# Performance work log

Hardware: AMD Instinct MI355X
Metric: run time of the kernel (lower is better)

Reference implementation:

```python
import jax, jax.numpy as jnp
import numpy as np

WINDOW = 512
OVERLAP = 64
STRIDE = WINDOW - OVERLAP  # 448
HEADS = 12
HEAD_DIM = 3072 // HEADS  # 256
SCALE = 1.0 / np.sqrt(HEAD_DIM)


def setup_inputs() -> dict:
    key = jax.random.key(0)
    ks = jax.random.split(key, 9)
    B, S, H = 1, 8192, 3072
    w = 0.02  # weight init scale
    return {
        "hidden_states": jax.random.normal(ks[0], (B, S, H), jnp.float32),
        "Wq": jax.random.normal(ks[1], (H, H), jnp.float32) * w,
        "bq": jnp.zeros((H,), jnp.float32),
        "Wk": jax.random.normal(ks[2], (H, H), jnp.float32) * w,
        "bk": jnp.zeros((H,), jnp.float32),
        "Wv": jax.random.normal(ks[3], (H, H), jnp.float32) * w,
        "bv": jnp.zeros((H,), jnp.float32),
        "Wo": jax.random.normal(ks[4], (H, H), jnp.float32) * w,
        "bo": jnp.zeros((H,), jnp.float32),
    }


def reference(hidden_states, Wq, bq, Wk, bk, Wv, bv, Wo, bo):
    B, S, H = hidden_states.shape
    n_win = -(-S // STRIDE)  # ceil: windows start at 0, STRIDE, 2*STRIDE, ... < S
    starts = np.arange(n_win) * STRIDE                      # static
    idx = starts[:, None] + np.arange(WINDOW)[None, :]      # [n_win, W]
    valid = jnp.asarray(idx < S)                            # [n_win, W] bool
    idx_c = np.minimum(idx, S - 1)                          # clamp for gather

    # Gather overlapping windows: [B, n_win, W, H] (redundant QKV on overlap, as in original)
    win = hidden_states[:, idx_c]

    def proj(Wm, bm):
        y = jnp.einsum('bnwh,oh->bnwo', win, Wm) + bm
        return y.reshape(B, n_win, WINDOW, HEADS, HEAD_DIM)

    q = proj(Wq, bq)
    k = proj(Wk, bk)
    v = proj(Wv, bv)

    scores = jnp.einsum('bnqhd,bnkhd->bnhqk', q, k) * SCALE  # [B,n_win,heads,W,W]
    # Padded (out-of-range) key positions of the short last window must not attend
    scores = jnp.where(valid[None, :, None, None, :], scores, -1e9)
    attn = jax.nn.softmax(scores, axis=-1)
    ctx = jnp.einsum('bnhqk,bnkhd->bnqhd', attn, v)
    ctx = ctx.reshape(B, n_win, WINDOW, H)
    out_w = jnp.einsum('bnwh,oh->bnwo', ctx, Wo) + bo        # [B,n_win,W,H]

    # zero padded query rows, then overlap-add + average
    out_w = out_w * valid[None, :, :, None].astype(out_w.dtype)
    flat_idx = jnp.asarray(idx_c.reshape(-1))                # [n_win*W]
    output = jnp.zeros((B, S, H), out_w.dtype).at[:, flat_idx].add(
        out_w.reshape(B, -1, H))
    counts = jnp.zeros((S,), out_w.dtype).at[flat_idx].add(
        valid.reshape(-1).astype(out_w.dtype))
    return output / jnp.maximum(counts, 1.0)[None, :, None]
```

## Files before the change

kernel.cpp:

```cpp
#include <hip/hip_runtime.h>
#include <hip/hip_bf16.h>
#include <stdint.h>

#define SEQ   8192
#define HDIM  3072
#define NWIN  19
#define WINL  512
#define STR   448
#define NHEAD 12
#define DHEAD 256
#define QKVN  9216
#define KVB   32
#define ATTN_SCALE 0.0625f

typedef unsigned short u16;
typedef __bf16 bf16x8 __attribute__((ext_vector_type(8)));
typedef float  f32x4  __attribute__((ext_vector_type(4)));
typedef unsigned short us8 __attribute__((ext_vector_type(8)));

__device__ __forceinline__ u16 f2b(float x) {
  return __builtin_bit_cast(u16, __float2bfloat16(x));
}
__device__ __forceinline__ float b2f(u16 u) {
  return __builtin_bit_cast(float, (unsigned int)(u) << 16);
}
__device__ __forceinline__ void gload_lds16(const void* g, void* l) {
  __builtin_amdgcn_global_load_lds(
      (const __attribute__((address_space(1))) void*)g,
      (__attribute__((address_space(3))) void*)l, 16, 0, 0);
}

__global__ __launch_bounds__(256) void cvt_f32_bf16(const float* __restrict__ src,
                                                    u16* __restrict__ dst, int n8) {
  int i = blockIdx.x * 256 + threadIdx.x;
  if (i >= n8) return;
  const float4* s4 = (const float4*)src;
  float4 a = s4[2 * i], b = s4[2 * i + 1];
  us8 o;
  o[0] = f2b(a.x); o[1] = f2b(a.y); o[2] = f2b(a.z); o[3] = f2b(a.w);
  o[4] = f2b(b.x); o[5] = f2b(b.y); o[6] = f2b(b.z); o[7] = f2b(b.w);
  *((us8*)dst + i) = o;
}

__global__ __launch_bounds__(256) void biascat(const float* __restrict__ bq,
                                               const float* __restrict__ bk,
                                               const float* __restrict__ bv,
                                               float* __restrict__ dst) {
  int i = blockIdx.x * 256 + threadIdx.x;
  if (i >= QKVN) return;
  dst[i] = (i < HDIM) ? bq[i] : ((i < 2 * HDIM) ? bk[i - HDIM] : bv[i - 2 * HDIM]);
}

template <bool BF16OUT>
__global__ __launch_bounds__(512, 2) void gemm256(const u16* __restrict__ A,
                                                  const u16* __restrict__ B,
                                                  const float* __restrict__ bias,
                                                  float* __restrict__ outF,
                                                  u16* __restrict__ outB,
                                                  u16* __restrict__ vtOut,
                                                  int N, int K) {
  __shared__ __align__(16) u16 As[2][2][128][64];
  __shared__ __align__(16) u16 Bs[2][2][128][64];
  const int tid = threadIdx.x;
  const int w = tid >> 6, l = tid & 63;
  const int wm = w >> 2, wn = w & 3;
  const int fr = l & 15, g = l >> 4;
  const int xcd = blockIdx.x & 7, loc = blockIdx.x >> 3;
  const int bn = loc >> 2, bm = xcd * 4 + (loc & 3);

  const int srow = tid >> 3;
  const int lc = (tid & 7) ^ ((tid >> 3) & 7);
  const u16* sA0 = A + (size_t)(bm * 256 + srow) * K + lc * 8;
  const u16* sA1 = sA0 + (size_t)64 * K;
  const u16* sB0 = B + (size_t)(bn * 256 + srow) * K + lc * 8;
  const u16* sB1 = sB0 + (size_t)64 * K;
  const size_t hiK = (size_t)128 * K;
  const int t16 = tid * 16;
  char* Aw = (char*)As;
  char* Bw = (char*)Bs;

  int rbA[4], rbB[2], ck[2];
#pragma unroll
  for (int i = 0; i < 4; ++i) rbA[i] = (i * 32 + wm * 16 + fr) * 128;
  rbB[0] = (wn * 16 + fr) * 128;
  rbB[1] = (64 + wn * 16 + fr) * 128;
  ck[0] = ((g) ^ (fr & 7)) * 16;
  ck[1] = ((4 + g) ^ (fr & 7)) * 16;

  f32x4 acc[8][4];
#pragma unroll
  for (int i = 0; i < 8; ++i)
#pragma unroll
    for (int j = 0; j < 4; ++j) acc[i][j] = (f32x4){0.f, 0.f, 0.f, 0.f};

  gload_lds16(sA0, Aw + t16); gload_lds16(sA1, Aw + 8192 + t16);
  gload_lds16(sB0, Bw + t16); gload_lds16(sB1, Bw + 8192 + t16);
  gload_lds16(sB0 + hiK, Bw + 16384 + t16); gload_lds16(sB1 + hiK, Bw + 16384 + 8192 + t16);
  gload_lds16(sA0 + hiK, Aw + 16384 + t16); gload_lds16(sA1 + hiK, Aw + 16384 + 8192 + t16);
  sA0 += 64; sA1 += 64; sB0 += 64; sB1 += 64;
  asm volatile("s_waitcnt vmcnt(4)" ::: "memory");
  __builtin_amdgcn_s_barrier();
  __builtin_amdgcn_sched_barrier(0);

  const int NT = K >> 6;
  for (int T = 0; T < NT; ++T) {
    const int cur = T & 1, pp = (T + 1) & 1;
    const bool ds = (T + 1 < NT);
    const bool last = (T == NT - 1);
    const char* ah = (const char*)As + cur * 32768;
    const char* bh = (const char*)Bs + cur * 32768;
    char* apw = Aw + pp * 32768;
    char* bpw = Bw + pp * 32768;
    bf16x8 af[4][2], bf[4][2];

#pragma unroll
    for (int mi = 0; mi < 4; ++mi)
#pragma unroll
      for (int kk = 0; kk < 2; ++kk)
        af[mi][kk] = *(const bf16x8*)(ah + rbA[mi] + ck[kk]);
#pragma unroll
    for (int ni = 0; ni < 2; ++ni)
#pragma unroll
      for (int kk = 0; kk < 2; ++kk)
        bf[ni][kk] = *(const bf16x8*)(bh + rbB[ni] + ck[kk]);
    if (ds) { gload_lds16(sA0, apw + t16); gload_lds16(sA1, apw + 8192 + t16); }
    __builtin_amdgcn_s_barrier();
    asm volatile("s_waitcnt lgkmcnt(0)" ::: "memory");
    __builtin_amdgcn_sched_barrier(0);
    __builtin_amdgcn_s_setprio(1);
#pragma unroll
    for (int kk = 0; kk < 2; ++kk)
#pragma unroll
      for (int mi = 0; mi < 4; ++mi)
#pragma unroll
        for (int ni = 0; ni < 2; ++ni)
          acc[mi][ni] = __builtin_amdgcn_mfma_f32_16x16x32_bf16(af[mi][kk], bf[ni][kk], acc[mi][ni], 0, 0, 0);
    __builtin_amdgcn_s_setprio(0);
    if (last) asm volatile("s_waitcnt vmcnt(2)" ::: "memory");
    else      asm volatile("s_waitcnt vmcnt(4)" ::: "memory");
    __builtin_amdgcn_s_barrier();

#pragma unroll
    for (int ni = 2; ni < 4; ++ni)
#pragma unroll
      for (int kk = 0; kk < 2; ++kk)
        bf[ni][kk] = *(const bf16x8*)(bh + 16384 + rbB[ni - 2] + ck[kk]);
    if (ds) { gload_lds16(sB0, bpw + t16); gload_lds16(sB1, bpw + 8192 + t16); }
    __builtin_amdgcn_s_barrier();
    asm volatile("s_waitcnt lgkmcnt(0)" ::: "memory");
    __builtin_amdgcn_sched_barrier(0);
    __builtin_amdgcn_s_setprio(1);
#pragma unroll
    for (int kk = 0; kk < 2; ++kk)
#pragma unroll
      for (int mi = 0; mi < 4; ++mi)
#pragma unroll
        for (int ni = 2; ni < 4; ++ni)
          acc[mi][ni] = __builtin_amdgcn_mfma_f32_16x16x32_bf16(af[mi][kk], bf[ni][kk], acc[mi][ni], 0, 0, 0);
    __builtin_amdgcn_s_setprio(0);
    if (last) asm volatile("s_waitcnt vmcnt(0)" ::: "memory");
    else      asm volatile("s_waitcnt vmcnt(4)" ::: "memory");
    __builtin_amdgcn_s_barrier();

#pragma unroll
    for (int mi = 0; mi < 4; ++mi)
#pragma unroll
      for (int kk = 0; kk < 2; ++kk)
        af[mi][kk] = *(const bf16x8*)(ah + 16384 + rbA[mi] + ck[kk]);
    if (ds) { gload_lds16(sB0 + hiK, bpw + 16384 + t16); gload_lds16(sB1 + hiK, bpw + 16384 + 8192 + t16); }
    __builtin_amdgcn_s_barrier();
    asm volatile("s_waitcnt lgkmcnt(0)" ::: "memory");
    __builtin_amdgcn_sched_barrier(0);
    __builtin_amdgcn_s_setprio(1);
#pragma unroll
    for (int kk = 0; kk < 2; ++kk)
#pragma unroll
      for (int mi = 0; mi < 4; ++mi)
#pragma unroll
        for (int ni = 0; ni < 2; ++ni)
          acc[mi + 4][ni] = __builtin_amdgcn_mfma_f32_16x16x32_bf16(af[mi][kk], bf[ni][kk], acc[mi + 4][ni], 0, 0, 0);
    __builtin_amdgcn_s_setprio(0);
    __builtin_amdgcn_s_barrier();

    if (ds) { gload_lds16(sA0 + hiK, apw + 16384 + t16); gload_lds16(sA1 + hiK, apw + 16384 + 8192 + t16); }
    __builtin_amdgcn_s_barrier();
    __builtin_amdgcn_s_setprio(1);
#pragma unroll
    for (int kk = 0; kk < 2; ++kk)
#pragma unroll
      for (int mi = 0; mi < 4; ++mi)
#pragma unroll
        for (int ni = 2; ni < 4; ++ni)
          acc[mi + 4][ni] = __builtin_amdgcn_mfma_f32_16x16x32_bf16(af[mi][kk], bf[ni][kk], acc[mi + 4][ni], 0, 0, 0);
    __builtin_amdgcn_s_setprio(0);
    if (!last) asm volatile("s_waitcnt vmcnt(4)" ::: "memory");
    __builtin_amdgcn_s_barrier();
    if (ds) { sA0 += 64; sA1 += 64; sB0 += 64; sB1 += 64; }
    __builtin_amdgcn_sched_barrier(0);
  }

#pragma unroll
  for (int ni = 0; ni < 4; ++ni) {
    const int c = bn * 256 + ni * 64 + wn * 16 + fr;
    const float bvv = bias ? bias[c] : 0.0f;
    const bool wv = BF16OUT && (vtOut != nullptr) && (c >= 2 * HDIM);
#pragma unroll
    for (int mi = 0; mi < 8; ++mi) {
      const int r0 = bm * 256 + mi * 32 + wm * 16 + g * 4;
      u16 t4[4];
#pragma unroll
      for (int jj = 0; jj < 4; ++jj) {
        float v = acc[mi][ni][jj] + bvv;
        if (BF16OUT) { u16 b_ = f2b(v); outB[(size_t)(r0 + jj) * N + c] = b_; t4[jj] = b_; }
        else         outF[(size_t)(r0 + jj) * N + c] = v;
      }
      if (wv) *(uint2*)(vtOut + (size_t)(c - 2 * HDIM) * SEQ + r0) = *(const uint2*)t4;
    }
  }
}

__global__ __launch_bounds__(256, 2) void attn_kernel(const u16* __restrict__ QKV,
                                                      const u16* __restrict__ Vt,
                                                      u16* __restrict__ ctxw) {
  __shared__ __align__(16) u16 Ks[2][KVB * 256];
  __shared__ __align__(16) u16 Vs[2][256 * KVB];
  __shared__ __align__(16) u16 Ps[4][16 * KVB];
  const int qb = blockIdx.x, h = blockIdx.y, n = blockIdx.z;
  const int tid = threadIdx.x, w = tid >> 6, l = tid & 63;
  const int g = l >> 4, fr = l & 15;
  const int s0 = n * STR;

  bf16x8 qf[8];
  {
    int sq = s0 + qb * 64 + w * 16 + fr;
    if (sq > SEQ - 1) sq = SEQ - 1;
    const u16* qbase = QKV + (size_t)sq * QKVN + h * DHEAD + g * 8;
#pragma unroll
    for (int dc = 0; dc < 8; ++dc) qf[dc] = *(const bf16x8*)(qbase + dc * 32);
  }
  f32x4 ctx[16];
#pragma unroll
  for (int dn = 0; dn < 16; ++dn) ctx[dn] = (f32x4){0.f, 0.f, 0.f, 0.f};
  float mrow[4] = {-3e38f, -3e38f, -3e38f, -3e38f};
  float lrow[4] = {0.f, 0.f, 0.f, 0.f};

  auto stage = [&](int kt) {
    const int sb = s0 + kt * KVB;
#pragma unroll
    for (int i = 0; i < 4; ++i) {
      const int c = i * 4 + w;
      {
        const int krow = c * 2 + (l >> 5);
        const int cl = (l & 31) ^ krow;
        int sk = sb + krow;
        if (sk > SEQ - 1) sk = SEQ - 1;
        gload_lds16(QKV + (size_t)sk * QKVN + HDIM + h * DHEAD + cl * 8,
                    (char*)&Ks[kt & 1][0] + c * 1024);
      }
      {
        const int d = c * 16 + (l >> 2);
        const int cl = (l & 3) ^ (d & 3) ^ ((d >> 2) & 3);
        int sv = sb + cl * 8;
        if (sv > SEQ - 8) sv = SEQ - 8;
        gload_lds16(Vt + (size_t)(h * DHEAD + d) * SEQ + sv,
                    (char*)&Vs[kt & 1][0] + c * 1024);
      }
    }
  };

  stage(0);
  const int mv = (fr & 3) ^ ((fr >> 2) & 3);
  char* pw = (char*)&Ps[w][0];

  for (int kt = 0; kt < 16; ++kt) {
    asm volatile("s_waitcnt vmcnt(0)" ::: "memory");
    __builtin_amdgcn_s_barrier();
    __builtin_amdgcn_sched_barrier(0);
    if (kt + 1 < 16) stage(kt + 1);
    const char* kb = (const char*)&Ks[kt & 1][0];
    const char* vb = (const char*)&Vs[kt & 1][0];
    const int sb = s0 + kt * KVB;

    f32x4 sacc[2];
#pragma unroll
    for (int kn = 0; kn < 2; ++kn) sacc[kn] = (f32x4){0.f, 0.f, 0.f, 0.f};
#pragma unroll
    for (int kn = 0; kn < 2; ++kn) {
      const int krow = kn * 16 + fr;
      const char* krp = kb + krow * 512;
#pragma unroll
      for (int dc = 0; dc < 8; ++dc) {
        bf16x8 kf = *(const bf16x8*)(krp + (((dc * 4 + g) ^ krow) << 4));
        sacc[kn] = __builtin_amdgcn_mfma_f32_16x16x32_bf16(qf[dc], kf, sacc[kn], 0, 0, 0);
      }
    }
    float mt[4];
#pragma unroll
    for (int kn = 0; kn < 2; ++kn) {
      const bool valid = (sb + kn * 16 + fr) < SEQ;
#pragma unroll
      for (int r = 0; r < 4; ++r) {
        float v = valid ? sacc[kn][r] * ATTN_SCALE : -1e9f;
        sacc[kn][r] = v;
        mt[r] = (kn == 0) ? v : fmaxf(mt[r], v);
      }
    }
#pragma unroll
    for (int r = 0; r < 4; ++r) {
#pragma unroll
      for (int off = 1; off < 16; off <<= 1)
        mt[r] = fmaxf(mt[r], __shfl_xor(mt[r], off, 64));
    }
    float corr[4];
#pragma unroll
    for (int r = 0; r < 4; ++r) {
      float mnew = fmaxf(mrow[r], mt[r]);
      corr[r] = __expf(mrow[r] - mnew);
      mrow[r] = mnew;
    }
    float psum[4] = {0.f, 0.f, 0.f, 0.f};
#pragma unroll
    for (int kn = 0; kn < 2; ++kn) {
#pragma unroll
      for (int r = 0; r < 4; ++r) {
        float p = __expf(sacc[kn][r] - mrow[r]);
        psum[r] += p;
        const int q = g * 4 + r;
        const int kv = kn * 16 + fr;
        *(u16*)(pw + q * 64 + ((((kv >> 3) ^ r ^ g) << 4) | ((2 * kv) & 15))) = f2b(p);
      }
    }
#pragma unroll
    for (int r = 0; r < 4; ++r) {
#pragma unroll
      for (int off = 1; off < 16; off <<= 1)
        psum[r] += __shfl_xor(psum[r], off, 64);
      lrow[r] = lrow[r] * corr[r] + psum[r];
    }
#pragma unroll
    for (int dn = 0; dn < 16; ++dn)
#pragma unroll
      for (int r = 0; r < 4; ++r) ctx[dn][r] *= corr[r];

    bf16x8 pf = *(const bf16x8*)(pw + fr * 64 + ((g ^ mv) << 4));
#pragma unroll
    for (int dn = 0; dn < 16; ++dn) {
      const int d = dn * 16 + fr;
      bf16x8 vf = *(const bf16x8*)(vb + d * 64 + ((g ^ mv) << 4));
      ctx[dn] = __builtin_amdgcn_mfma_f32_16x16x32_bf16(pf, vf, ctx[dn], 0, 0, 0);
    }
  }
  float inv[4];
#pragma unroll
  for (int r = 0; r < 4; ++r) inv[r] = 1.0f / lrow[r];
  const int qrow0 = qb * 64 + w * 16 + g * 4;
#pragma unroll
  for (int dn = 0; dn < 16; ++dn) {
#pragma unroll
    for (int r = 0; r < 4; ++r) {
      ctxw[(size_t)(n * WINL + qrow0 + r) * HDIM + h * DHEAD + dn * 16 + fr] =
          f2b(ctx[dn][r] * inv[r]);
    }
  }
}

__global__ __launch_bounds__(256) void combine_kernel(const u16* __restrict__ ctxw,
                                                      u16* __restrict__ ctx_avg) {
  int idx = blockIdx.x * 256 + threadIdx.x;
  if (idx >= SEQ * (HDIM / 8)) return;
  const int s = idx / (HDIM / 8);
  const int cc = (idx % (HDIM / 8)) * 8;
  const int w1 = s / STR;
  const int off1 = s - w1 * STR;
  us8 a = *(const us8*)(ctxw + (size_t)(w1 * WINL + off1) * HDIM + cc);
  if (w1 >= 1 && off1 < (WINL - STR)) {
    us8 b = *(const us8*)(ctxw + (size_t)((w1 - 1) * WINL + off1 + STR) * HDIM + cc);
#pragma unroll
    for (int j = 0; j < 8; ++j) a[j] = f2b(0.5f * (b2f(a[j]) + b2f(b[j])));
  }
  *(us8*)(ctx_avg + (size_t)s * HDIM + cc) = a;
}

__global__ void ws_marker(float* out, float v) { out[0] = v; }

extern "C" void kernel_launch(void* const* d_in, const int* in_sizes, int n_in,
                              void* d_out, int out_size, void* d_ws, size_t ws_size,
                              hipStream_t stream) {
  const float* X  = (const float*)d_in[0];
  const float* Wq = (const float*)d_in[1];
  const float* bq = (const float*)d_in[2];
  const float* Wk = (const float*)d_in[3];
  const float* bk = (const float*)d_in[4];
  const float* Wv = (const float*)d_in[5];
  const float* bv = (const float*)d_in[6];
  const float* Wo = (const float*)d_in[7];
  const float* bo = (const float*)d_in[8];
  float* out = (float*)d_out;

  const size_t OFF_XB   = 0;
  const size_t OFF_WQKV = 50331648;
  const size_t OFF_WO   = 106954752;
  const size_t OFF_QKV  = 125829120;
  const size_t OFF_VT   = 276824064;
  const size_t OFF_BIAS = 327155712;
  const size_t WS_NEED  = 327192576;
  if (ws_size < WS_NEED) {
    hipMemsetAsync(d_out, 0, (size_t)out_size * 4, stream);
    ws_marker<<<1, 1, 0, stream>>>(out, (float)(ws_size / 1048576));
    return;
  }
  char* ws = (char*)d_ws;
  u16* Xb      = (u16*)(ws + OFF_XB);
  u16* Wqkvb   = (u16*)(ws + OFF_WQKV);
  u16* Wob     = (u16*)(ws + OFF_WO);
  u16* QKV     = (u16*)(ws + OFF_QKV);
  u16* Vt      = (u16*)(ws + OFF_VT);
  float* biasQ = (float*)(ws + OFF_BIAS);
  u16* ctxw    = (u16*)d_out;
  u16* ctx_avg = Xb;

  cvt_f32_bf16<<<12288, 256, 0, stream>>>(X, Xb, SEQ * HDIM / 8);
  cvt_f32_bf16<<<4608, 256, 0, stream>>>(Wq, Wqkvb, HDIM * HDIM / 8);
  cvt_f32_bf16<<<4608, 256, 0, stream>>>(Wk, Wqkvb + (size_t)HDIM * HDIM, HDIM * HDIM / 8);
  cvt_f32_bf16<<<4608, 256, 0, stream>>>(Wv, Wqkvb + (size_t)2 * HDIM * HDIM, HDIM * HDIM / 8);
  cvt_f32_bf16<<<4608, 256, 0, stream>>>(Wo, Wob, HDIM * HDIM / 8);
  biascat<<<36, 256, 0, stream>>>(bq, bk, bv, biasQ);

  gemm256<true><<<dim3((SEQ / 256) * (QKVN / 256)), 512, 0, stream>>>(
      Xb, Wqkvb, biasQ, nullptr, QKV, Vt, QKVN, HDIM);

  attn_kernel<<<dim3(8, NHEAD, NWIN), 256, 0, stream>>>(QKV, Vt, ctxw);

  combine_kernel<<<12288, 256, 0, stream>>>(ctxw, ctx_avg);

  gemm256<false><<<dim3((SEQ / 256) * (HDIM / 256)), 512, 0, stream>>>(
      ctx_avg, Wob, bo, out, nullptr, nullptr, HDIM, HDIM);
}
```

Baseline: 903.2 us.

## Read attention K/V directly from global, widen KV tile, lazily rescale softmax

The attention kernel drops its double-buffered LDS staging of K and V tiles and the per-tile block barriers. Each wave now loads K rows and transposed V rows straight from global memory into MFMA operands, processing 64 keys per step instead of 32. It also skips the online-softmax rescale of the max, sum and context accumulators unless some score exceeds the running max by more than 8. Occupancy is raised to 3 blocks per CU now that LDS use is small. The trade-off is redundant global/L2 reads across the four waves and unbounded-by-max probabilities (up to e^8) in bf16.

```diff
diff --git a/kernel.cpp b/kernel.cpp
--- a/kernel.cpp
+++ b/kernel.cpp
@@ -10,7 +10,6 @@
 #define NHEAD 12
 #define DHEAD 256
 #define QKVN  9216
-#define KVB   32
 #define ATTN_SCALE 0.0625f
 
 typedef unsigned short u16;
@@ -219,12 +218,10 @@
   }
 }
 
-__global__ __launch_bounds__(256, 2) void attn_kernel(const u16* __restrict__ QKV,
+__global__ __launch_bounds__(256, 3) void attn_kernel(const u16* __restrict__ QKV,
                                                       const u16* __restrict__ Vt,
                                                       u16* __restrict__ ctxw) {
-  __shared__ __align__(16) u16 Ks[2][KVB * 256];
-  __shared__ __align__(16) u16 Vs[2][256 * KVB];
-  __shared__ __align__(16) u16 Ps[4][16 * KVB];
+  __shared__ __align__(16) u16 Ps[4][16 * 64];
   const int qb = blockIdx.x, h = blockIdx.y, n = blockIdx.z;
   const int tid = threadIdx.x, w = tid >> 6, l = tid & 63;
   const int g = l >> 4, fr = l & 15;
@@ -244,90 +241,68 @@
   float mrow[4] = {-3e38f, -3e38f, -3e38f, -3e38f};
   float lrow[4] = {0.f, 0.f, 0.f, 0.f};
 
-  auto stage = [&](int kt) {
-    const int sb = s0 + kt * KVB;
-#pragma unroll
-    for (int i = 0; i < 4; ++i) {
-      const int c = i * 4 + w;
-      {
-        const int krow = c * 2 + (l >> 5);
-        const int cl = (l & 31) ^ krow;
-        int sk = sb + krow;
-        if (sk > SEQ - 1) sk = SEQ - 1;
-        gload_lds16(QKV + (size_t)sk * QKVN + HDIM + h * DHEAD + cl * 8,
-                    (char*)&Ks[kt & 1][0] + c * 1024);
-      }
-      {
-        const int d = c * 16 + (l >> 2);
-        const int cl = (l & 3) ^ (d & 3) ^ ((d >> 2) & 3);
-        int sv = sb + cl * 8;
-        if (sv > SEQ - 8) sv = SEQ - 8;
-        gload_lds16(Vt + (size_t)(h * DHEAD + d) * SEQ + sv,
-                    (char*)&Vs[kt & 1][0] + c * 1024);
-      }
-    }
-  };
-
-  stage(0);
-  const int mv = (fr & 3) ^ ((fr >> 2) & 3);
+  const u16* kbase = QKV + HDIM + h * DHEAD;
+  const u16* vbase = Vt + (size_t)(h * DHEAD) * SEQ;
   char* pw = (char*)&Ps[w][0];
 
-  for (int kt = 0; kt < 16; ++kt) {
-    asm volatile("s_waitcnt vmcnt(0)" ::: "memory");
-    __builtin_amdgcn_s_barrier();
-    __builtin_amdgcn_sched_barrier(0);
-    if (kt + 1 < 16) stage(kt + 1);
-    const char* kb = (const char*)&Ks[kt & 1][0];
-    const char* vb = (const char*)&Vs[kt & 1][0];
-    const int sb = s0 + kt * KVB;
-
-    f32x4 sacc[2];
-#pragma unroll
-    for (int kn = 0; kn < 2; ++kn) sacc[kn] = (f32x4){0.f, 0.f, 0.f, 0.f};
-#pragma unroll
-    for (int kn = 0; kn < 2; ++kn) {
-      const int krow = kn * 16 + fr;
-      const char* krp = kb + krow * 512;
+  for (int kt = 0; kt < 8; ++kt) {
+    const int sb = s0 + kt * 64;
+    const int sbc = (sb > SEQ - 64) ? (SEQ - 64) : sb;
+
+    f32x4 sacc[4];
+#pragma unroll
+    for (int kn = 0; kn < 4; ++kn) sacc[kn] = (f32x4){0.f, 0.f, 0.f, 0.f};
+#pragma unroll
+    for (int kn = 0; kn < 4; ++kn) {
+      int sk = sb + kn * 16 + fr;
+      if (sk > SEQ - 1) sk = SEQ - 1;
+      const u16* kr = kbase + (size_t)sk * QKVN;
 #pragma unroll
       for (int dc = 0; dc < 8; ++dc) {
-        bf16x8 kf = *(const bf16x8*)(krp + (((dc * 4 + g) ^ krow) << 4));
+        bf16x8 kf = *(const bf16x8*)(kr + (dc * 4 + g) * 8);
         sacc[kn] = __builtin_amdgcn_mfma_f32_16x16x32_bf16(qf[dc], kf, sacc[kn], 0, 0, 0);
       }
     }
-    float mt[4];
-#pragma unroll
-    for (int kn = 0; kn < 2; ++kn) {
+    bool ok = true;
+#pragma unroll
+    for (int kn = 0; kn < 4; ++kn) {
       const bool valid = (sb + kn * 16 + fr) < SEQ;
 #pragma unroll
       for (int r = 0; r < 4; ++r) {
         float v = valid ? sacc[kn][r] * ATTN_SCALE : -1e9f;
         sacc[kn][r] = v;
-        mt[r] = (kn == 0) ? v : fmaxf(mt[r], v);
-      }
-    }
-#pragma unroll
-    for (int r = 0; r < 4; ++r) {
-#pragma unroll
-      for (int off = 1; off < 16; off <<= 1)
-        mt[r] = fmaxf(mt[r], __shfl_xor(mt[r], off, 64));
-    }
-    float corr[4];
-#pragma unroll
-    for (int r = 0; r < 4; ++r) {
-      float mnew = fmaxf(mrow[r], mt[r]);
-      corr[r] = __expf(mrow[r] - mnew);
-      mrow[r] = mnew;
+        ok = ok && (v <= mrow[r] + 8.0f);
+      }
+    }
+    if (!__all(ok)) {
+      float mt[4];
+#pragma unroll
+      for (int kn = 0; kn < 4; ++kn)
+#pragma unroll
+        for (int r = 0; r < 4; ++r)
+          mt[r] = (kn == 0) ? sacc[0][r] : fmaxf(mt[r], sacc[kn][r]);
+#pragma unroll
+      for (int r = 0; r < 4; ++r) {
+#pragma unroll
+        for (int off = 1; off < 16; off <<= 1)
+          mt[r] = fmaxf(mt[r], __shfl_xor(mt[r], off, 64));
+        float mnew = fmaxf(mrow[r], mt[r]);
+        float corr = __expf(mrow[r] - mnew);
+        mrow[r] = mnew;
+        lrow[r] *= corr;
+#pragma unroll
+        for (int dn = 0; dn < 16; ++dn) ctx[dn][r] *= corr;
+      }
     }
     float psum[4] = {0.f, 0.f, 0.f, 0.f};
 #pragma unroll
-    for (int kn = 0; kn < 2; ++kn) {
+    for (int kn = 0; kn < 4; ++kn) {
 #pragma unroll
       for (int r = 0; r < 4; ++r) {
         float p = __expf(sacc[kn][r] - mrow[r]);
         psum[r] += p;
         const int q = g * 4 + r;
-        const int kv = kn * 16 + fr;
-        *(u16*)(pw + q * 64 + ((((kv >> 3) ^ r ^ g) << 4) | ((2 * kv) & 15))) = f2b(p);
+        *(u16*)(pw + q * 128 + ((2 * (kn * 16 + fr)) ^ ((q & 7) << 4))) = f2b(p);
       }
     }
 #pragma unroll
@@ -335,19 +310,23 @@
 #pragma unroll
       for (int off = 1; off < 16; off <<= 1)
         psum[r] += __shfl_xor(psum[r], off, 64);
-      lrow[r] = lrow[r] * corr[r] + psum[r];
-    }
-#pragma unroll
-    for (int dn = 0; dn < 16; ++dn)
-#pragma unroll
-      for (int r = 0; r < 4; ++r) ctx[dn][r] *= corr[r];
-
-    bf16x8 pf = *(const bf16x8*)(pw + fr * 64 + ((g ^ mv) << 4));
+      lrow[r] += psum[r];
+    }
+    asm volatile("s_waitcnt lgkmcnt(0)" ::: "memory");
+    __builtin_amdgcn_sched_barrier(0);
+
+    bf16x8 pf[2];
+#pragma unroll
+    for (int kc = 0; kc < 2; ++kc)
+      pf[kc] = *(const bf16x8*)(pw + fr * 128 + ((kc * 64 + g * 16) ^ ((fr & 7) << 4)));
 #pragma unroll
     for (int dn = 0; dn < 16; ++dn) {
-      const int d = dn * 16 + fr;
-      bf16x8 vf = *(const bf16x8*)(vb + d * 64 + ((g ^ mv) << 4));
-      ctx[dn] = __builtin_amdgcn_mfma_f32_16x16x32_bf16(pf, vf, ctx[dn], 0, 0, 0);
+      const u16* vr = vbase + (size_t)(dn * 16 + fr) * SEQ + sbc;
+#pragma unroll
+      for (int kc = 0; kc < 2; ++kc) {
+        bf16x8 vf = *(const bf16x8*)(vr + (kc * 4 + g) * 8);
+        ctx[dn] = __builtin_amdgcn_mfma_f32_16x16x32_bf16(pf[kc], vf, ctx[dn], 0, 0, 0);
+      }
     }
   }
   float inv[4];
```

After: 1.230 ms. 1.36x slower.
